# Kernel optimization log

Measured on AMD Instinct MI355X. Metric: run time of the kernel, lower is better.

## Reference

```python
import jax, jax.numpy as jnp
import numpy as np

HIDDEN = 128

def setup_inputs() -> dict:
    key = jax.random.key(0)
    k1, k2, k3 = jax.random.split(key, 3)
    B, T, D = 64, 2048, 128
    scale_x = 1.0 / np.sqrt(D)
    scale_h = 1.0 / np.sqrt(HIDDEN)
    return {
        "x": jax.random.normal(k1, (B, T, D), dtype=jnp.float32),
        "Wx": jax.random.normal(k2, (D, 4 * HIDDEN), dtype=jnp.float32) * scale_x,
        "Wh": jax.random.normal(k3, (HIDDEN, 4 * HIDDEN), dtype=jnp.float32) * scale_h,
        "b": jnp.zeros((4 * HIDDEN,), dtype=jnp.float32),
    }

def reference(x, Wx, Wh, b):
    # x: [B, T, D] (batch_first). Unrolled LSTM, zero initial states.
    B, T, D = x.shape
    H = Wh.shape[0]
    # Precompute input projections for all timesteps: [T, B, 4H]
    xg = jnp.einsum('btd,dg->tbg', x, Wx) + b

    def step(carry, xg_t):
        h, c = carry
        gates = xg_t + h @ Wh  # [B, 4H]
        i, f, g, o = jnp.split(gates, 4, axis=-1)
        i = jax.nn.sigmoid(i)
        f = jax.nn.sigmoid(f)
        g = jnp.tanh(g)
        o = jax.nn.sigmoid(o)
        c_new = f * c + i * g
        h_new = o * jnp.tanh(c_new)
        return (h_new, c_new), (h_new, c_new)

    h0 = jnp.zeros((B, H), dtype=x.dtype)
    c0 = jnp.zeros((B, H), dtype=x.dtype)
    _, (hs, cs) = jax.lax.scan(step, (h0, c0), xg)
    # [T, B, H] -> [B, T, H] to match torch batch_first layout
    return hs.transpose(1, 0, 2), cs.transpose(1, 0, 2)
```

## Files before the change

kernel.cpp:

```cpp
#include <hip/hip_runtime.h>
#include <hip/hip_bf16.h>


#define B_ 64
#define T_ 2048
#define D_ 128
#define H_ 128
#define G_ 512

typedef __bf16 v8bf __attribute__((ext_vector_type(8)));
typedef float f32x4 __attribute__((ext_vector_type(4)));

__device__ __forceinline__ float fast_exp2(float x) { return __builtin_amdgcn_exp2f(x); }
__device__ __forceinline__ float fast_rcp(float x)  { return __builtin_amdgcn_rcpf(x); }
__device__ __forceinline__ float sigmoid_(float x) {
    return fast_rcp(1.0f + fast_exp2(x * -1.44269504088896341f));
}
__device__ __forceinline__ float tanh_(float x) {
    return 1.0f - 2.0f * fast_rcp(1.0f + fast_exp2(x * 2.88539008177792682f));
}
__device__ __forceinline__ unsigned short f2bf(float f) {
    union { float f; unsigned u; } v; v.f = f;
    unsigned r = v.u + 0x7FFFu + ((v.u >> 16) & 1u);
    return (unsigned short)(r >> 16);
}

__global__ void __launch_bounds__(256)
wxt_kernel(const float* __restrict__ Wx, unsigned short* __restrict__ wxt) {
    int t = blockIdx.x * 256 + threadIdx.x;
    int col = t >> 4;
    int k0  = (t & 15) * 8;
    union { unsigned short s[8]; v8bf v; } u;
#pragma unroll
    for (int j = 0; j < 8; ++j) u.s[j] = f2bf(Wx[(size_t)(k0 + j) * G_ + col]);
    *(v8bf*)&wxt[(size_t)col * D_ + k0] = u.v;
}

__device__ __forceinline__ void gemm32(const float* __restrict__ x,
                                       const unsigned short* __restrict__ wxt,
                                       const float* __restrict__ bias,
                                       float* __restrict__ xg,
                                       int t0g, int Cg, int gb, int tid) {
    const int lane = tid & 63;
    const int q    = lane >> 4;
    const int cl   = lane & 15;
    const int kb   = q * 8;
    const int wave = tid >> 6;
    const int half = wave >> 2;
    const int w4   = wave & 3;
    const int rowg = gb * 32 + half * 16;
    const int b    = rowg / Cg;
    const int tl   = rowg - b * Cg;

    const float* xr = x + ((size_t)b * T_ + (size_t)(t0g + tl) + cl) * D_;
    v8bf af[4];
#pragma unroll
    for (int kk = 0; kk < 4; ++kk) {
        float4 lo = *(const float4*)&xr[kk * 32 + kb];
        float4 hi = *(const float4*)&xr[kk * 32 + kb + 4];
        union { unsigned u[4]; v8bf v; } pk;
        asm("v_cvt_pk_bf16_f32 %0, %1, %2" : "=v"(pk.u[0]) : "v"(lo.x), "v"(lo.y));
        asm("v_cvt_pk_bf16_f32 %0, %1, %2" : "=v"(pk.u[1]) : "v"(lo.z), "v"(lo.w));
        asm("v_cvt_pk_bf16_f32 %0, %1, %2" : "=v"(pk.u[2]) : "v"(hi.x), "v"(hi.y));
        asm("v_cvt_pk_bf16_f32 %0, %1, %2" : "=v"(pk.u[3]) : "v"(hi.z), "v"(hi.w));
        af[kk] = pk.v;
    }

    f32x4 acc[8];
#pragma unroll
    for (int n = 0; n < 8; ++n) {
        float bv = bias[w4 * 128 + n * 16 + cl];
        acc[n] = (f32x4){bv, bv, bv, bv};
    }
#pragma unroll
    for (int kk = 0; kk < 4; ++kk) {
#pragma unroll
        for (int n = 0; n < 8; ++n) {
            v8bf bf = *(const v8bf*)&wxt[(size_t)(w4 * 128 + n * 16 + cl) * D_ + kk * 32 + kb];
            acc[n] = __builtin_amdgcn_mfma_f32_16x16x32_bf16(af[kk], bf, acc[n], 0, 0, 0);
        }
    }
#pragma unroll
    for (int n = 0; n < 8; ++n) {
        int hu = n * 16 + cl;
#pragma unroll
        for (int r = 0; r < 4; ++r)
            xg[(size_t)(rowg + q * 4 + r) * G_ + hu * 4 + w4] = acc[n][r];
    }
}

__global__ void __launch_bounds__(512)
xg_gemm512(const float* __restrict__ x, const unsigned short* __restrict__ wxt,
           const float* __restrict__ bias, float* __restrict__ xg,
           int t0g, int Cg) {
    gemm32(x, wxt, bias, xg, t0g, Cg, blockIdx.x, threadIdx.x);
}

__global__ void __launch_bounds__(512)
__attribute__((amdgpu_waves_per_eu(2, 2)))
lstm_fused(const float* __restrict__ x, const unsigned short* __restrict__ wxt,
           const float* __restrict__ Wh, const float* __restrict__ bias,
           float* __restrict__ hs, float* __restrict__ cs,
           float* __restrict__ hstate, float* __restrict__ cstate,
           const float* __restrict__ xgCur, float* __restrict__ xgNext,
           int t0, int C, int t0n, int Cn) {
    const int tid  = threadIdx.x;
    const int lane = tid & 63;
    const int q    = lane >> 4;
    const int cl   = lane & 15;
    const int kb   = q * 8;

    if (blockIdx.x >= 64) {
        gemm32(x, wxt, bias, xgNext, t0n, Cn, blockIdx.x - 64, tid);
        return;
    }

    const int b  = blockIdx.x;
    const int w  = tid >> 6;
    const int hu = w * 16 + cl;

    __shared__ __align__(16) unsigned short h_u16[2][H_];

    v8bf whf[4][4];
#pragma unroll
    for (int kk = 0; kk < 4; ++kk) {
#pragma unroll
        for (int gc = 0; gc < 4; ++gc) {
            union { unsigned short s[8]; v8bf v; } uw;
#pragma unroll
            for (int j = 0; j < 8; ++j)
                uw.s[j] = f2bf(Wh[(size_t)(kk * 32 + kb + j) * G_ + gc * 128 + hu]);
            whf[kk][gc] = uw.v;
        }
    }

    float c = 0.0f;
    if (t0 > 0) c = cstate[b * H_ + hu];
    if (tid < H_) h_u16[0][tid] = f2bf((t0 > 0) ? hstate[b * H_ + tid] : 0.0f);
    __syncthreads();

    const float* xgb = xgCur + (size_t)b * C * G_;

    f32x4 xp0 = *(const f32x4*)&xgb[(size_t)0 * G_ + hu * 4];
    f32x4 xp1 = *(const f32x4*)&xgb[(size_t)1 * G_ + hu * 4];
    f32x4 xp2 = *(const f32x4*)&xgb[(size_t)2 * G_ + hu * 4];
    f32x4 xp3 = *(const f32x4*)&xgb[(size_t)3 * G_ + hu * 4];

#define RNN_STEP(PX, TCUR, PR, PW)                                             \
    {                                                                          \
        f32x4 a0 = {0.f, 0.f, 0.f, 0.f};                                       \
        f32x4 a1 = {0.f, 0.f, 0.f, 0.f};                                       \
        f32x4 a2 = {0.f, 0.f, 0.f, 0.f};                                       \
        f32x4 a3 = {0.f, 0.f, 0.f, 0.f};                                       \
        _Pragma("unroll")                                                      \
        for (int kk = 0; kk < 4; ++kk) {                                       \
            v8bf ha = *(const v8bf*)&h_u16[PR][kk * 32 + kb];                  \
            a0 = __builtin_amdgcn_mfma_f32_16x16x32_bf16(ha, whf[kk][0], a0, 0, 0, 0); \
            a1 = __builtin_amdgcn_mfma_f32_16x16x32_bf16(ha, whf[kk][1], a1, 0, 0, 0); \
            a2 = __builtin_amdgcn_mfma_f32_16x16x32_bf16(ha, whf[kk][2], a2, 0, 0, 0); \
            a3 = __builtin_amdgcn_mfma_f32_16x16x32_bf16(ha, whf[kk][3], a3, 0, 0, 0); \
        }                                                                      \
        float iv = sigmoid_(a0[0] + PX.x);                                     \
        float fv = sigmoid_(a1[0] + PX.y);                                     \
        float gv = tanh_(a2[0] + PX.z);                                        \
        float ov = sigmoid_(a3[0] + PX.w);                                     \
        c = fmaf(fv, c, iv * gv);                                              \
        float hnv = ov * tanh_(c);                                             \
        { int pf = ((TCUR) + 4 < C) ? ((TCUR) + 4) : (C - 1);                  \
          PX = *(const f32x4*)&xgb[(size_t)pf * G_ + hu * 4]; }                \
        if (q == 0) {                                                          \
            h_u16[PW][hu] = f2bf(hnv);                                         \
            size_t off = ((size_t)b * T_ + (size_t)(t0 + (TCUR))) * H_ + hu;   \
            hs[off] = hnv; cs[off] = c;                                        \
        }                                                                      \
        asm volatile("s_waitcnt lgkmcnt(0)\n\ts_barrier" ::: "memory");        \
    }

#undef RNN_STEP
#define RNN_STEP(PX, TCUR, PR, PW)                                             \
    {                                                                          \
        f32x4 a0 = {0.f, 0.f, 0.f, 0.f};                                       \
        f32x4 a1 = {0.f, 0.f, 0.f, 0.f};                                       \
        f32x4 a2 = {0.f, 0.f, 0.f, 0.f};                                       \
        f32x4 a3 = {0.f, 0.f, 0.f, 0.f};                                       \
        _Pragma("unroll")                                                      \
        for (int kk = 0; kk < 4; ++kk) {                                       \
            v8bf ha = *(const v8bf*)&h_u16[PR][kk * 32 + kb];                  \
            a0 = __builtin_amdgcn_mfma_f32_16x16x32_bf16(ha, whf[kk][0], a0, 0, 0, 0); \
            a1 = __builtin_amdgcn_mfma_f32_16x16x32_bf16(ha, whf[kk][1], a1, 0, 0, 0); \
            a2 = __builtin_amdgcn_mfma_f32_16x16x32_bf16(ha, whf[kk][2], a2, 0, 0, 0); \
            a3 = __builtin_amdgcn_mfma_f32_16x16x32_bf16(ha, whf[kk][3], a3, 0, 0, 0); \
        }                                                                      \
        float iv = sigmoid_(a0[0] + PX[0]);                                    \
        float fv = sigmoid_(a1[0] + PX[1]);                                    \
        float gv = tanh_(a2[0] + PX[2]);                                       \
        float ov = sigmoid_(a3[0] + PX[3]);                                    \
        c = fmaf(fv, c, iv * gv);                                              \
        float hnv = ov * tanh_(c);                                             \
        { int pf = ((TCUR) + 4 < C) ? ((TCUR) + 4) : (C - 1);                  \
          PX = *(const f32x4*)&xgb[(size_t)pf * G_ + hu * 4]; }                \
        if (q == 0) {                                                          \
            h_u16[PW][hu] = f2bf(hnv);                                         \
            size_t off = ((size_t)b * T_ + (size_t)(t0 + (TCUR))) * H_ + hu;   \
            hs[off] = hnv; cs[off] = c;                                        \
        }                                                                      \
        asm volatile("s_waitcnt lgkmcnt(0)\n\ts_barrier" ::: "memory");        \
    }

#pragma unroll 1
    for (int t = 0; t < C; t += 4) {
        RNN_STEP(xp0, t,     0, 1)
        RNN_STEP(xp1, t + 1, 1, 0)
        RNN_STEP(xp2, t + 2, 0, 1)
        RNN_STEP(xp3, t + 3, 1, 0)
    }
#undef RNN_STEP

    if (q == 0) cstate[b * H_ + hu] = c;
    if (tid < H_) {
        unsigned ui = ((unsigned)h_u16[0][tid]) << 16;
        float hf; __builtin_memcpy(&hf, &ui, 4);
        hstate[b * H_ + tid] = hf;
    }
}

extern "C" void kernel_launch(void* const* d_in, const int* in_sizes, int n_in,
                              void* d_out, int out_size, void* d_ws, size_t ws_size,
                              hipStream_t stream) {
    const float* x    = (const float*)d_in[0];
    const float* Wx   = (const float*)d_in[1];
    const float* Wh   = (const float*)d_in[2];
    const float* bias = (const float*)d_in[3];

    float* hs = (float*)d_out;
    float* cs = hs + (size_t)B_ * T_ * H_;

    float* hstate = (float*)d_ws;
    float* cstate = hstate + B_ * H_;
    unsigned short* wxt = (unsigned short*)(cstate + B_ * H_);
    float* xgA = (float*)(wxt + (size_t)G_ * D_);

    const size_t head_bytes = (size_t)2 * B_ * H_ * 4 + (size_t)G_ * D_ * 2;
    size_t avail = (ws_size > head_bytes) ? (ws_size - head_bytes) : 0;
    const size_t bytes_per_t = (size_t)B_ * G_ * sizeof(float);

    int C = (int)(avail / (2 * bytes_per_t));
    if (C > 512) C = 512;
    C &= ~63;
    if (C < 64) C = 64;

    float* xgB = xgA + (size_t)B_ * C * G_;

    wxt_kernel<<<32, 256, 0, stream>>>(Wx, wxt);

    int nChunks = 0, t0s[64], Cis[64];
    for (int t0 = 0; t0 < T_; t0 += C) {
        t0s[nChunks] = t0;
        Cis[nChunks] = (T_ - t0 < C) ? (T_ - t0) : C;
        ++nChunks;
    }

    xg_gemm512<<<(B_ * Cis[0]) / 32, 512, 0, stream>>>(x, wxt, bias, xgA, t0s[0], Cis[0]);

    for (int i = 0; i < nChunks; ++i) {
        float* bufCur  = (i & 1) ? xgB : xgA;
        float* bufNext = (i & 1) ? xgA : xgB;
        int hasNext = (i + 1 < nChunks);
        int t0n = hasNext ? t0s[i + 1] : 0;
        int Cn  = hasNext ? Cis[i + 1] : 64;
        int nGemm = hasNext ? (B_ * Cn) / 32 : 0;
        lstm_fused<<<64 + nGemm, 512, 0, stream>>>(
            x, wxt, Wh, bias, hs, cs, hstate, cstate,
            bufCur, bufNext, t0s[i], Cis[i], t0n, Cn);
    }
}
```

Measured before the change: 956.5 us.

## Halve LSTM block to 4 waves, each wave computing two hidden-unit groups

Shrinks the recurrent block from 512 to 256 threads, so each wave processes two 16-unit slices of every gate with twice the MFMAs per step. The aim is to cut barrier and synchronisation overhead across waves in the serial time loop. The companion xg GEMM blocks are also reduced to 256 threads with 16 rows each. In exchange, per-wave MFMA latency and register use roughly double, and the prefetch distance shrinks from 4 steps to 2.

```diff
diff --git a/kernel.cpp b/kernel.cpp
--- a/kernel.cpp
+++ b/kernel.cpp
@@ -36,7 +36,7 @@
     *(v8bf*)&wxt[(size_t)col * D_ + k0] = u.v;
 }
 
-__device__ __forceinline__ void gemm32(const float* __restrict__ x,
+__device__ __forceinline__ void gemm16(const float* __restrict__ x,
                                        const unsigned short* __restrict__ wxt,
                                        const float* __restrict__ bias,
                                        float* __restrict__ xg,
@@ -45,10 +45,8 @@
     const int q    = lane >> 4;
     const int cl   = lane & 15;
     const int kb   = q * 8;
-    const int wave = tid >> 6;
-    const int half = wave >> 2;
-    const int w4   = wave & 3;
-    const int rowg = gb * 32 + half * 16;
+    const int g4   = tid >> 6;
+    const int rowg = gb * 16;
     const int b    = rowg / Cg;
     const int tl   = rowg - b * Cg;
 
@@ -69,35 +67,35 @@
     f32x4 acc[8];
 #pragma unroll
     for (int n = 0; n < 8; ++n) {
-        float bv = bias[w4 * 128 + n * 16 + cl];
+        float bv = bias[g4 * 128 + n * 16 + cl];
         acc[n] = (f32x4){bv, bv, bv, bv};
     }
 #pragma unroll
     for (int kk = 0; kk < 4; ++kk) {
 #pragma unroll
         for (int n = 0; n < 8; ++n) {
-            v8bf bf = *(const v8bf*)&wxt[(size_t)(w4 * 128 + n * 16 + cl) * D_ + kk * 32 + kb];
+            v8bf bf = *(const v8bf*)&wxt[(size_t)(g4 * 128 + n * 16 + cl) * D_ + kk * 32 + kb];
             acc[n] = __builtin_amdgcn_mfma_f32_16x16x32_bf16(af[kk], bf, acc[n], 0, 0, 0);
         }
     }
 #pragma unroll
     for (int n = 0; n < 8; ++n) {
-        int hu = n * 16 + cl;
+        int u = n * 16 + cl;
 #pragma unroll
         for (int r = 0; r < 4; ++r)
-            xg[(size_t)(rowg + q * 4 + r) * G_ + hu * 4 + w4] = acc[n][r];
-    }
-}
-
-__global__ void __launch_bounds__(512)
-xg_gemm512(const float* __restrict__ x, const unsigned short* __restrict__ wxt,
+            xg[(size_t)(rowg + q * 4 + r) * G_ + u * 4 + g4] = acc[n][r];
+    }
+}
+
+__global__ void __launch_bounds__(256)
+xg_gemm256(const float* __restrict__ x, const unsigned short* __restrict__ wxt,
            const float* __restrict__ bias, float* __restrict__ xg,
            int t0g, int Cg) {
-    gemm32(x, wxt, bias, xg, t0g, Cg, blockIdx.x, threadIdx.x);
-}
-
-__global__ void __launch_bounds__(512)
-__attribute__((amdgpu_waves_per_eu(2, 2)))
+    gemm16(x, wxt, bias, xg, t0g, Cg, blockIdx.x, threadIdx.x);
+}
+
+__global__ void __launch_bounds__(256)
+__attribute__((amdgpu_waves_per_eu(1, 1)))
 lstm_fused(const float* __restrict__ x, const unsigned short* __restrict__ wxt,
            const float* __restrict__ Wh, const float* __restrict__ bias,
            float* __restrict__ hs, float* __restrict__ cs,
@@ -111,112 +109,97 @@
     const int kb   = q * 8;
 
     if (blockIdx.x >= 64) {
-        gemm32(x, wxt, bias, xgNext, t0n, Cn, blockIdx.x - 64, tid);
+        gemm16(x, wxt, bias, xgNext, t0n, Cn, blockIdx.x - 64, tid);
         return;
     }
 
     const int b  = blockIdx.x;
     const int w  = tid >> 6;
-    const int hu = w * 16 + cl;
+    const int u0 = w * 32 + cl;
+    const int u1 = u0 + 16;
 
     __shared__ __align__(16) unsigned short h_u16[2][H_];
 
-    v8bf whf[4][4];
+    v8bf whf[4][8];
 #pragma unroll
     for (int kk = 0; kk < 4; ++kk) {
 #pragma unroll
-        for (int gc = 0; gc < 4; ++gc) {
-            union { unsigned short s[8]; v8bf v; } uw;
-#pragma unroll
-            for (int j = 0; j < 8; ++j)
-                uw.s[j] = f2bf(Wh[(size_t)(kk * 32 + kb + j) * G_ + gc * 128 + hu]);
-            whf[kk][gc] = uw.v;
+        for (int g = 0; g < 4; ++g) {
+#pragma unroll
+            for (int half = 0; half < 2; ++half) {
+                union { unsigned short s[8]; v8bf v; } uw;
+                int col = g * 128 + w * 32 + half * 16 + cl;
+#pragma unroll
+                for (int j = 0; j < 8; ++j)
+                    uw.s[j] = f2bf(Wh[(size_t)(kk * 32 + kb + j) * G_ + col]);
+                whf[kk][g * 2 + half] = uw.v;
+            }
         }
     }
 
-    float c = 0.0f;
-    if (t0 > 0) c = cstate[b * H_ + hu];
+    float c0 = 0.0f, c1 = 0.0f;
+    if (t0 > 0) { c0 = cstate[b * H_ + u0]; c1 = cstate[b * H_ + u1]; }
     if (tid < H_) h_u16[0][tid] = f2bf((t0 > 0) ? hstate[b * H_ + tid] : 0.0f);
     __syncthreads();
 
     const float* xgb = xgCur + (size_t)b * C * G_;
 
-    f32x4 xp0 = *(const f32x4*)&xgb[(size_t)0 * G_ + hu * 4];
-    f32x4 xp1 = *(const f32x4*)&xgb[(size_t)1 * G_ + hu * 4];
-    f32x4 xp2 = *(const f32x4*)&xgb[(size_t)2 * G_ + hu * 4];
-    f32x4 xp3 = *(const f32x4*)&xgb[(size_t)3 * G_ + hu * 4];
-
-#define RNN_STEP(PX, TCUR, PR, PW)                                             \
+    f32x4 xA0 = *(const f32x4*)&xgb[(size_t)0 * G_ + u0 * 4];
+    f32x4 xA1 = *(const f32x4*)&xgb[(size_t)0 * G_ + u1 * 4];
+    f32x4 xB0 = *(const f32x4*)&xgb[(size_t)1 * G_ + u0 * 4];
+    f32x4 xB1 = *(const f32x4*)&xgb[(size_t)1 * G_ + u1 * 4];
+
+#define RNN_STEP(PX0, PX1, TCUR, PR, PW)                                       \
     {                                                                          \
-        f32x4 a0 = {0.f, 0.f, 0.f, 0.f};                                       \
-        f32x4 a1 = {0.f, 0.f, 0.f, 0.f};                                       \
-        f32x4 a2 = {0.f, 0.f, 0.f, 0.f};                                       \
-        f32x4 a3 = {0.f, 0.f, 0.f, 0.f};                                       \
+        f32x4 a00 = {0,0,0,0}, a01 = {0,0,0,0};                                \
+        f32x4 a10 = {0,0,0,0}, a11 = {0,0,0,0};                                \
+        f32x4 a20 = {0,0,0,0}, a21 = {0,0,0,0};                                \
+        f32x4 a30 = {0,0,0,0}, a31 = {0,0,0,0};                                \
         _Pragma("unroll")                                                      \
         for (int kk = 0; kk < 4; ++kk) {                                       \
             v8bf ha = *(const v8bf*)&h_u16[PR][kk * 32 + kb];                  \
-            a0 = __builtin_amdgcn_mfma_f32_16x16x32_bf16(ha, whf[kk][0], a0, 0, 0, 0); \
-            a1 = __builtin_amdgcn_mfma_f32_16x16x32_bf16(ha, whf[kk][1], a1, 0, 0, 0); \
-            a2 = __builtin_amdgcn_mfma_f32_16x16x32_bf16(ha, whf[kk][2], a2, 0, 0, 0); \
-            a3 = __builtin_amdgcn_mfma_f32_16x16x32_bf16(ha, whf[kk][3], a3, 0, 0, 0); \
+            a00 = __builtin_amdgcn_mfma_f32_16x16x32_bf16(ha, whf[kk][0], a00, 0, 0, 0); \
+            a01 = __builtin_amdgcn_mfma_f32_16x16x32_bf16(ha, whf[kk][1], a01, 0, 0, 0); \
+            a10 = __builtin_amdgcn_mfma_f32_16x16x32_bf16(ha, whf[kk][2], a10, 0, 0, 0); \
+            a11 = __builtin_amdgcn_mfma_f32_16x16x32_bf16(ha, whf[kk][3], a11, 0, 0, 0); \
+            a20 = __builtin_amdgcn_mfma_f32_16x16x32_bf16(ha, whf[kk][4], a20, 0, 0, 0); \
+            a21 = __builtin_amdgcn_mfma_f32_16x16x32_bf16(ha, whf[kk][5], a21, 0, 0, 0); \
+            a30 = __builtin_amdgcn_mfma_f32_16x16x32_bf16(ha, whf[kk][6], a30, 0, 0, 0); \
+            a31 = __builtin_amdgcn_mfma_f32_16x16x32_bf16(ha, whf[kk][7], a31, 0, 0, 0); \
         }                                                                      \
-        float iv = sigmoid_(a0[0] + PX.x);                                     \
-        float fv = sigmoid_(a1[0] + PX.y);                                     \
-        float gv = tanh_(a2[0] + PX.z);                                        \
-        float ov = sigmoid_(a3[0] + PX.w);                                     \
-        c = fmaf(fv, c, iv * gv);                                              \
-        float hnv = ov * tanh_(c);                                             \
-        { int pf = ((TCUR) + 4 < C) ? ((TCUR) + 4) : (C - 1);                  \
-          PX = *(const f32x4*)&xgb[(size_t)pf * G_ + hu * 4]; }                \
+        float iv0 = sigmoid_(a00[0] + PX0[0]);                                 \
+        float fv0 = sigmoid_(a10[0] + PX0[1]);                                 \
+        float gv0 = tanh_(a20[0] + PX0[2]);                                    \
+        float ov0 = sigmoid_(a30[0] + PX0[3]);                                 \
+        float iv1 = sigmoid_(a01[0] + PX1[0]);                                 \
+        float fv1 = sigmoid_(a11[0] + PX1[1]);                                 \
+        float gv1 = tanh_(a21[0] + PX1[2]);                                    \
+        float ov1 = sigmoid_(a31[0] + PX1[3]);                                 \
+        c0 = fmaf(fv0, c0, iv0 * gv0);                                         \
+        c1 = fmaf(fv1, c1, iv1 * gv1);                                         \
+        float h0v = ov0 * tanh_(c0);                                           \
+        float h1v = ov1 * tanh_(c1);                                           \
+        { int pf = ((TCUR) + 2 < C) ? ((TCUR) + 2) : (C - 1);                  \
+          PX0 = *(const f32x4*)&xgb[(size_t)pf * G_ + u0 * 4];                 \
+          PX1 = *(const f32x4*)&xgb[(size_t)pf * G_ + u1 * 4]; }               \
         if (q == 0) {                                                          \
-            h_u16[PW][hu] = f2bf(hnv);                                         \
-            size_t off = ((size_t)b * T_ + (size_t)(t0 + (TCUR))) * H_ + hu;   \
-            hs[off] = hnv; cs[off] = c;                                        \
+            h_u16[PW][u0] = f2bf(h0v);                                         \
+            h_u16[PW][u1] = f2bf(h1v);                                         \
+            size_t off = ((size_t)b * T_ + (size_t)(t0 + (TCUR))) * H_ + u0;   \
+            hs[off] = h0v;      cs[off] = c0;                                  \
+            hs[off + 16] = h1v; cs[off + 16] = c1;                             \
         }                                                                      \
         asm volatile("s_waitcnt lgkmcnt(0)\n\ts_barrier" ::: "memory");        \
     }
 
+#pragma unroll 1
+    for (int t = 0; t < C; t += 2) {
+        RNN_STEP(xA0, xA1, t,     0, 1)
+        RNN_STEP(xB0, xB1, t + 1, 1, 0)
+    }
 #undef RNN_STEP
-#define RNN_STEP(PX, TCUR, PR, PW)                                             \
-    {                                                                          \
-        f32x4 a0 = {0.f, 0.f, 0.f, 0.f};                                       \
-        f32x4 a1 = {0.f, 0.f, 0.f, 0.f};                                       \
-        f32x4 a2 = {0.f, 0.f, 0.f, 0.f};                                       \
-        f32x4 a3 = {0.f, 0.f, 0.f, 0.f};                                       \
-        _Pragma("unroll")                                                      \
-        for (int kk = 0; kk < 4; ++kk) {                                       \
-            v8bf ha = *(const v8bf*)&h_u16[PR][kk * 32 + kb];                  \
-            a0 = __builtin_amdgcn_mfma_f32_16x16x32_bf16(ha, whf[kk][0], a0, 0, 0, 0); \
-            a1 = __builtin_amdgcn_mfma_f32_16x16x32_bf16(ha, whf[kk][1], a1, 0, 0, 0); \
-            a2 = __builtin_amdgcn_mfma_f32_16x16x32_bf16(ha, whf[kk][2], a2, 0, 0, 0); \
-            a3 = __builtin_amdgcn_mfma_f32_16x16x32_bf16(ha, whf[kk][3], a3, 0, 0, 0); \
-        }                                                                      \
-        float iv = sigmoid_(a0[0] + PX[0]);                                    \
-        float fv = sigmoid_(a1[0] + PX[1]);                                    \
-        float gv = tanh_(a2[0] + PX[2]);                                       \
-        float ov = sigmoid_(a3[0] + PX[3]);                                    \
-        c = fmaf(fv, c, iv * gv);                                              \
-        float hnv = ov * tanh_(c);                                             \
-        { int pf = ((TCUR) + 4 < C) ? ((TCUR) + 4) : (C - 1);                  \
-          PX = *(const f32x4*)&xgb[(size_t)pf * G_ + hu * 4]; }                \
-        if (q == 0) {                                                          \
-            h_u16[PW][hu] = f2bf(hnv);                                         \
-            size_t off = ((size_t)b * T_ + (size_t)(t0 + (TCUR))) * H_ + hu;   \
-            hs[off] = hnv; cs[off] = c;                                        \
-        }                                                                      \
-        asm volatile("s_waitcnt lgkmcnt(0)\n\ts_barrier" ::: "memory");        \
-    }
-
-#pragma unroll 1
-    for (int t = 0; t < C; t += 4) {
-        RNN_STEP(xp0, t,     0, 1)
-        RNN_STEP(xp1, t + 1, 1, 0)
-        RNN_STEP(xp2, t + 2, 0, 1)
-        RNN_STEP(xp3, t + 3, 1, 0)
-    }
-#undef RNN_STEP
-
-    if (q == 0) cstate[b * H_ + hu] = c;
+
+    if (q == 0) { cstate[b * H_ + u0] = c0; cstate[b * H_ + u1] = c1; }
     if (tid < H_) {
         unsigned ui = ((unsigned)h_u16[0][tid]) << 16;
         float hf; __builtin_memcpy(&hf, &ui, 4);
@@ -260,7 +243,7 @@
         ++nChunks;
     }
 
-    xg_gemm512<<<(B_ * Cis[0]) / 32, 512, 0, stream>>>(x, wxt, bias, xgA, t0s[0], Cis[0]);
+    xg_gemm256<<<(B_ * Cis[0]) / 16, 256, 0, stream>>>(x, wxt, bias, xgA, t0s[0], Cis[0]);
 
     for (int i = 0; i < nChunks; ++i) {
         float* bufCur  = (i & 1) ? xgB : xgA;
@@ -268,8 +251,8 @@
         int hasNext = (i + 1 < nChunks);
         int t0n = hasNext ? t0s[i + 1] : 0;
         int Cn  = hasNext ? Cis[i + 1] : 64;
-        int nGemm = hasNext ? (B_ * Cn) / 32 : 0;
-        lstm_fused<<<64 + nGemm, 512, 0, stream>>>(
+        int nGemm = hasNext ? (B_ * Cn) / 16 : 0;
+        lstm_fused<<<64 + nGemm, 256, 0, stream>>>(
             x, wxt, Wh, bias, hs, cs, hstate, cstate,
             bufCur, bufNext, t0s[i], Cis[i], t0n, Cn);
     }
```

Result: slower. 1.187 ms (+24.1%).
